# Performance work log

Hardware: AMD Instinct MI355X
Metric: run time of the kernel (lower is better)

The kernel has to match this reference:

```python
import jax, jax.numpy as jnp
import numpy as np

E = 1024      # emb_dim
H = 16        # num_heads
DH = E // H   # per-head atten_dim
B = 2
T = 2048


def _layernorm(x, scale, shift, eps=1e-5):
    mean = x.mean(axis=-1, keepdims=True)
    var = ((x - mean) ** 2).mean(axis=-1, keepdims=True)  # unbiased=False
    return scale * (x - mean) / jnp.sqrt(var + eps) + shift


def _gelu(x):
    # Faithful to source: tanh(sqrt(2/pi)*x + 0.044715*x^3)  (no sqrt on cubic term)
    c = jnp.sqrt(jnp.asarray(2.0 / jnp.pi, x.dtype))
    return 0.5 * x * (1.0 + jnp.tanh(c * x + 0.044715 * x ** 3))


def setup_inputs() -> dict:
    key = jax.random.key(0)
    ks = jax.random.split(key, 12)
    s = 0.02
    return {
        "x":     jax.random.normal(ks[0], (B, T, E), jnp.float32),
        "Wq":    jax.random.normal(ks[1], (H, E, DH), jnp.float32) * s,
        "Wk":    jax.random.normal(ks[2], (H, E, DH), jnp.float32) * s,
        "Wv":    jax.random.normal(ks[3], (H, E, DH), jnp.float32) * s,
        "fc_w":  jax.random.normal(ks[4], (E, E), jnp.float32) * s,
        "fc_b":  jnp.zeros((E,), jnp.float32),
        "ln1_s": jnp.ones((E,), jnp.float32),
        "ln1_b": jnp.zeros((E,), jnp.float32),
        "ln2_s": jnp.ones((E,), jnp.float32),
        "ln2_b": jnp.zeros((E,), jnp.float32),
        "ff_w1": jax.random.normal(ks[5], (E, 4 * E), jnp.float32) * s,
        "ff_b1": jnp.zeros((4 * E,), jnp.float32),
        "ff_w2": jax.random.normal(ks[6], (4 * E, E), jnp.float32) * s,
        "ff_b2": jnp.zeros((E,), jnp.float32),
    }


def _attention(x, Wq, Wk, Wv, fc_w, fc_b):
    b, t, _ = x.shape
    q = jnp.einsum("bte,hed->bhtd", x, Wq)
    k = jnp.einsum("bte,hed->bhtd", x, Wk)
    v = jnp.einsum("bte,hed->bhtd", x, Wv)
    scores = jnp.einsum("bhtd,bhsd->bhts", q, k)
    causal = jnp.triu(jnp.ones((t, t), bool), 1)
    scores = jnp.where(causal, -jnp.inf, scores)
    w = jax.nn.softmax(scores / jnp.sqrt(jnp.asarray(DH, x.dtype)), axis=-1)
    ctx = jnp.einsum("bhts,bhsd->bhtd", w, v)
    # faithful quirk from source: per-head transpose(1,2) then reshape(b, T, d_out)
    ctx = jnp.swapaxes(ctx, 2, 3).reshape(b, H, t, DH)
    concat = ctx.transpose(0, 2, 1, 3).reshape(b, t, E)
    return concat @ fc_w + fc_b


def reference(x, Wq, Wk, Wv, fc_w, fc_b, ln1_s, ln1_b, ln2_s, ln2_b,
              ff_w1, ff_b1, ff_w2, ff_b2):
    h = _attention(_layernorm(x, ln1_s, ln1_b), Wq, Wk, Wv, fc_w, fc_b) + x
    y = _layernorm(h, ln2_s, ln2_b)
    y = _gelu(y @ ff_w1 + ff_b1) @ ff_w2 + ff_b2
    return y + h
```

## Files before the change

kernel.cpp:

```cpp
#include <hip/hip_runtime.h>


#define En 1024
#define Hn 16
#define DHn 64
#define Bn 2
#define Tn 2048
#define Mrows 4096

typedef __attribute__((ext_vector_type(8))) short bf16x8;
typedef __attribute__((ext_vector_type(4))) float f32x4;

__device__ __forceinline__ short f2bf(float f) {
    unsigned u = __float_as_uint(f);
    u += 0x7FFFu + ((u >> 16) & 1u);
    return (short)(u >> 16);
}
__device__ __forceinline__ ushort f2bfu(float f) {
    unsigned u = __float_as_uint(f);
    u += 0x7FFFu + ((u >> 16) & 1u);
    return (ushort)(u >> 16);
}
__device__ __forceinline__ float bf2f(ushort u) {
    return __uint_as_float((unsigned)u << 16);
}
__device__ __forceinline__ unsigned cvt_pk_bf16(float lo, float hi) {
    unsigned r;
    asm("v_cvt_pk_bf16_f32 %0, %1, %2" : "=v"(r) : "v"(lo), "v"(hi));
    return r;
}

__device__ __forceinline__ float gelu_f(float x) {
    float u = 0.79788456080286535588f * x + 0.044715f * x * x * x;
    float t = __expf(2.0f * u);
    return x * t / (t + 1.0f);
}

__device__ __forceinline__ void load_lds16(const void* g, void* l) {
    __builtin_amdgcn_global_load_lds(
        (const __attribute__((address_space(1))) unsigned int*)(uintptr_t)g,
        (__attribute__((address_space(3))) unsigned int*)(uintptr_t)l,
        16, 0, 0);
}

__global__ __launch_bounds__(256) void ln_kernel(
    const float* __restrict__ in, const float* __restrict__ sc,
    const float* __restrict__ sh, ushort* __restrict__ out)
{
    int row = blockIdx.x;
    int tid = threadIdx.x;
    float4 v = ((const float4*)(in + (size_t)row * En))[tid];
    float s  = v.x + v.y + v.z + v.w;
    float s2 = v.x*v.x + v.y*v.y + v.z*v.z + v.w*v.w;
    #pragma unroll
    for (int off = 32; off > 0; off >>= 1) {
        s  += __shfl_down(s,  off);
        s2 += __shfl_down(s2, off);
    }
    __shared__ float red[2][4];
    int wave = tid >> 6, lane = tid & 63;
    if (lane == 0) { red[0][wave] = s; red[1][wave] = s2; }
    __syncthreads();
    s  = red[0][0] + red[0][1] + red[0][2] + red[0][3];
    s2 = red[1][0] + red[1][1] + red[1][2] + red[1][3];
    float mean = s * (1.0f / En);
    float var  = s2 * (1.0f / En) - mean * mean;
    float r = rsqrtf(var + 1e-5f);
    float4 scv = ((const float4*)sc)[tid];
    float4 shv = ((const float4*)sh)[tid];
    ushort4 o;
    o.x = f2bfu(scv.x * (v.x - mean) * r + shv.x);
    o.y = f2bfu(scv.y * (v.y - mean) * r + shv.y);
    o.z = f2bfu(scv.z * (v.z - mean) * r + shv.z);
    o.w = f2bfu(scv.w * (v.w - mean) * r + shv.w);
    ((ushort4*)(out + (size_t)row * En))[tid] = o;
}

__global__ __launch_bounds__(256) void ln2_fuse(
    const ushort* __restrict__ P0, const ushort* __restrict__ P1,
    const float* __restrict__ bias, const float* __restrict__ x,
    const float* __restrict__ sc, const float* __restrict__ sh,
    ushort* __restrict__ hb, ushort* __restrict__ ynb)
{
    int row = blockIdx.x, tid = threadIdx.x;
    size_t idx = (size_t)row * 256 + tid;
    ushort4 a = ((const ushort4*)P0)[idx];
    ushort4 b = ((const ushort4*)P1)[idx];
    float4 bi = ((const float4*)bias)[tid];
    float4 xr = ((const float4*)x)[idx];
    float4 v;
    v.x = bf2f(a.x) + bf2f(b.x) + bi.x + xr.x;
    v.y = bf2f(a.y) + bf2f(b.y) + bi.y + xr.y;
    v.z = bf2f(a.z) + bf2f(b.z) + bi.z + xr.z;
    v.w = bf2f(a.w) + bf2f(b.w) + bi.w + xr.w;
    ushort4 hv;
    hv.x = f2bfu(v.x); hv.y = f2bfu(v.y); hv.z = f2bfu(v.z); hv.w = f2bfu(v.w);
    ((ushort4*)hb)[idx] = hv;
    float s  = v.x + v.y + v.z + v.w;
    float s2 = v.x*v.x + v.y*v.y + v.z*v.z + v.w*v.w;
    #pragma unroll
    for (int off = 32; off > 0; off >>= 1) {
        s  += __shfl_down(s,  off);
        s2 += __shfl_down(s2, off);
    }
    __shared__ float red[2][4];
    int wave = tid >> 6, lane = tid & 63;
    if (lane == 0) { red[0][wave] = s; red[1][wave] = s2; }
    __syncthreads();
    s  = red[0][0] + red[0][1] + red[0][2] + red[0][3];
    s2 = red[1][0] + red[1][1] + red[1][2] + red[1][3];
    float mean = s * (1.0f / En);
    float var  = s2 * (1.0f / En) - mean * mean;
    float r = rsqrtf(var + 1e-5f);
    float4 scv = ((const float4*)sc)[tid];
    float4 shv = ((const float4*)sh)[tid];
    ushort4 o;
    o.x = f2bfu(scv.x * (v.x - mean) * r + shv.x);
    o.y = f2bfu(scv.y * (v.y - mean) * r + shv.y);
    o.z = f2bfu(scv.z * (v.z - mean) * r + shv.z);
    o.w = f2bfu(scv.w * (v.w - mean) * r + shv.w);
    ((ushort4*)ynb)[idx] = o;
}

__global__ __launch_bounds__(256) void ff2_reduce4(
    const ushort* __restrict__ P, const float* __restrict__ bias,
    const ushort* __restrict__ hb, float* __restrict__ out)
{
    int tid = threadIdx.x;
    size_t i = (size_t)blockIdx.x * 256 + tid;
    const size_t S = (size_t)Mrows * En / 4;
    ushort4 a = ((const ushort4*)P)[i];
    ushort4 b = ((const ushort4*)P)[i + S];
    ushort4 c = ((const ushort4*)P)[i + 2 * S];
    ushort4 d = ((const ushort4*)P)[i + 3 * S];
    float4 bi = ((const float4*)bias)[tid];
    ushort4 hu = ((const ushort4*)hb)[i];
    float4 o;
    o.x = (bf2f(a.x) + bf2f(b.x)) + (bf2f(c.x) + bf2f(d.x)) + bi.x + bf2f(hu.x);
    o.y = (bf2f(a.y) + bf2f(b.y)) + (bf2f(c.y) + bf2f(d.y)) + bi.y + bf2f(hu.y);
    o.z = (bf2f(a.z) + bf2f(b.z)) + (bf2f(c.z) + bf2f(d.z)) + bi.z + bf2f(hu.z);
    o.w = (bf2f(a.w) + bf2f(b.w)) + (bf2f(c.w) + bf2f(d.w)) + bi.w + bf2f(hu.w);
    ((float4*)out)[i] = o;
}

__global__ __launch_bounds__(256) void prep_w(
    const float* __restrict__ Wq, const float* __restrict__ Wk,
    const float* __restrict__ Wv, const float* __restrict__ fc_w,
    const float* __restrict__ ff_w1, const float* __restrict__ ff_w2,
    ushort* __restrict__ wqkv, ushort* __restrict__ wfc,
    ushort* __restrict__ wf1, ushort* __restrict__ wf2)
{
    int bid = blockIdx.x;
    const float* in; ushort* out; int N, ldo, k0, n0;
    if (bid < 768) {
        int z = bid >> 4, kb = bid & 15;
        int sel = z / 16, h = z % 16;
        in  = (sel == 0 ? Wq : sel == 1 ? Wk : Wv) + (size_t)h * En * DHn;
        out = wqkv + (size_t)(sel * 1024 + h * 64) * En;
        N = DHn; ldo = En; k0 = kb * 64; n0 = 0;
    } else if (bid < 1024) {
        int b2 = bid - 768;
        in = fc_w; out = wfc; N = En; ldo = En;
        k0 = (b2 & 15) * 64; n0 = (b2 >> 4) * 64;
    } else if (bid < 2048) {
        int b2 = bid - 1024;
        in = ff_w1; out = wf1; N = 4 * En; ldo = En;
        k0 = (b2 & 15) * 64; n0 = (b2 >> 4) * 64;
    } else {
        int b2 = bid - 2048;
        in = ff_w2; out = wf2; N = En; ldo = 4 * En;
        k0 = (b2 & 63) * 64; n0 = (b2 >> 6) * 64;
    }
    __shared__ float t[64][65];
    int tid = threadIdx.x, r = tid >> 4, c4 = (tid & 15) * 4;
    #pragma unroll
    for (int i = 0; i < 4; ++i) {
        float4 v = *(const float4*)(in + (size_t)(k0 + r + i * 16) * N + n0 + c4);
        t[r + i * 16][c4 + 0] = v.x; t[r + i * 16][c4 + 1] = v.y;
        t[r + i * 16][c4 + 2] = v.z; t[r + i * 16][c4 + 3] = v.w;
    }
    __syncthreads();
    #pragma unroll
    for (int i = 0; i < 4; ++i) {
        int n = r + i * 16;
        ushort4 u;
        u.x = f2bfu(t[c4 + 0][n]); u.y = f2bfu(t[c4 + 1][n]);
        u.z = f2bfu(t[c4 + 2][n]); u.w = f2bfu(t[c4 + 3][n]);
        *(ushort4*)(out + (size_t)(n0 + n) * ldo + k0 + c4) = u;
    }
}

template<int MODE, int TN>
__global__ __launch_bounds__(256) void gemm_bf16(
    const ushort* __restrict__ A, int lda,
    const ushort* __restrict__ Bt, int ldb, int Kloop,
    const float* __restrict__ bias,
    ushort* __restrict__ Cb, int ldc,
    ushort* __restrict__ qo, ushort* __restrict__ ko, ushort* __restrict__ vo)
{
    constexpr int WCN = TN / 2;
    constexpr int NI  = WCN / 16;
    constexpr int BIW = TN * 8 / 256;
    constexpr int STAGE = 128 * 64 + TN * 64;
    constexpr int BOUNCE = (MODE == 2 || MODE == 1) ? 4 * 64 * 68
                         : (MODE == 3 ? 128 * 68 : 0);
    constexpr int SMEMN = STAGE > BOUNCE ? STAGE : BOUNCE;
    __shared__ ushort smem[SMEMN];
    ushort* As = smem;
    ushort* Bs = smem + 128 * 64;
    int tid = threadIdx.x, wv = tid >> 6, lid = tid & 63;
    int m0 = blockIdx.x * 128, n0 = blockIdx.y * TN;
    int koff = blockIdx.z * Kloop;
    int wr = wv >> 1, wc = wv & 1;
    int hm = lid & 15, hk = lid >> 4;

    f32x4 acc[4][NI];
    #pragma unroll
    for (int i = 0; i < 4; ++i)
        #pragma unroll
        for (int j = 0; j < NI; ++j) acc[i][j] = (f32x4){0.f, 0.f, 0.f, 0.f};

    const ushort* Abase = A + (size_t)m0 * lda + koff;
    const ushort* Bbase = Bt + (size_t)n0 * ldb + koff;

    for (int k0 = 0; k0 < Kloop; k0 += 64) {
        __syncthreads();
        #pragma unroll
        for (int i = 0; i < 4; ++i) {
            int c = wv * 256 + i * 64 + lid;
            int r = c >> 3, s = c & 7;
            int j = s ^ (r & 7);
            load_lds16(Abase + (size_t)r * lda + k0 + j * 8,
                       &As[(wv * 256 + i * 64) * 8]);
        }
        #pragma unroll
        for (int i = 0; i < BIW; ++i) {
            int c = wv * (BIW * 64) + i * 64 + lid;
            int r = c >> 3, s = c & 7;
            int j = s ^ (r & 7);
            load_lds16(Bbase + (size_t)r * ldb + k0 + j * 8,
                       &Bs[(wv * (BIW * 64) + i * 64) * 8]);
        }
        __syncthreads();
        #pragma unroll
        for (int kk = 0; kk < 2; ++kk) {
            bf16x8 af[4], bfr[NI];
            #pragma unroll
            for (int mi = 0; mi < 4; ++mi) {
                int r = wr * 64 + mi * 16 + hm;
                int slot = ((kk << 2) | hk) ^ (r & 7);
                af[mi] = *(const bf16x8*)&As[(r * 8 + slot) * 8];
            }
            #pragma unroll
            for (int ni = 0; ni < NI; ++ni) {
                int r = wc * WCN + ni * 16 + hm;
                int slot = ((kk << 2) | hk) ^ (r & 7);
                bfr[ni] = *(const bf16x8*)&Bs[(r * 8 + slot) * 8];
            }
            #pragma unroll
            for (int mi = 0; mi < 4; ++mi)
                #pragma unroll
                for (int ni = 0; ni < NI; ++ni)
                    acc[mi][ni] = __builtin_amdgcn_mfma_f32_16x16x32_bf16(
                        af[mi], bfr[ni], acc[mi][ni], 0, 0, 0);
        }
    }

    int colbase = n0 + wc * WCN + hm;
    if (MODE == 1) {
        __syncthreads();
        ushort* Ls = smem + wv * (64 * 68);
        #pragma unroll
        for (int ni = 0; ni < NI; ++ni) {
            int col = colbase + ni * 16;
            float bb = bias[col];
            #pragma unroll
            for (int mi = 0; mi < 4; ++mi)
                #pragma unroll
                for (int r = 0; r < 4; ++r)
                    Ls[(mi * 16 + hk * 4 + r) * 68 + ni * 16 + hm] =
                        f2bfu(gelu_f(acc[mi][ni][r] + bb));
        }
        ushort* outp = Cb + (size_t)(m0 + wr * 64) * ldc + n0 + wc * 64;
        int dcol = hm * 4;
        #pragma unroll
        for (int i = 0; i < 16; ++i) {
            int t = hk + i * 4;
            *(ushort4*)(outp + (size_t)t * ldc + dcol) =
                *(const ushort4*)&Ls[t * 68 + dcol];
        }
    } else if (MODE == 2) {
        __syncthreads();
        ushort* Ls = smem + wv * (64 * 68);
        int col0 = n0 + wc * 64;
        int sel = col0 >> 10, h = (col0 & 1023) >> 6;
        if (sel < 2) {
            #pragma unroll
            for (int ni = 0; ni < NI; ++ni)
                #pragma unroll
                for (int mi = 0; mi < 4; ++mi)
                    #pragma unroll
                    for (int r = 0; r < 4; ++r)
                        Ls[(mi * 16 + hk * 4 + r) * 68 + ni * 16 + hm] =
                            f2bfu(acc[mi][ni][r]);
            ushort* outp = (sel == 0 ? qo : ko) + (size_t)h * (Mrows * DHn);
            int dcol = hm * 4;
            #pragma unroll
            for (int i = 0; i < 16; ++i) {
                int t = hk + i * 4;
                *(ushort4*)(outp + (size_t)(m0 + wr * 64 + t) * DHn + dcol) =
                    *(const ushort4*)&Ls[t * 68 + dcol];
            }
        } else {
            #pragma unroll
            for (int ni = 0; ni < NI; ++ni)
                #pragma unroll
                for (int mi = 0; mi < 4; ++mi)
                    #pragma unroll
                    for (int r = 0; r < 4; ++r)
                        Ls[(ni * 16 + hm) * 68 + mi * 16 + hk * 4 + r] =
                            f2bfu(acc[mi][ni][r]);
            int bb2 = m0 >> 11;
            int t0 = (m0 & 2047) + wr * 64;
            ushort* outp = vo + ((size_t)((h * 2 + bb2) * 64)) * Tn + t0;
            int tcol = hm * 4;
            #pragma unroll
            for (int i = 0; i < 16; ++i) {
                int d = hk + i * 4;
                *(ushort4*)(outp + (size_t)d * Tn + tcol) =
                    *(const ushort4*)&Ls[d * 68 + tcol];
            }
        }
    } else {
        __syncthreads();
        ushort* Ls = smem;
        #pragma unroll
        for (int ni = 0; ni < NI; ++ni)
            #pragma unroll
            for (int mi = 0; mi < 4; ++mi)
                #pragma unroll
                for (int r = 0; r < 4; ++r)
                    Ls[(wr * 64 + mi * 16 + hk * 4 + r) * 68
                       + wc * WCN + ni * 16 + hm] = f2bfu(acc[mi][ni][r]);
        __syncthreads();
        ushort* Cp = Cb + (size_t)blockIdx.z * Mrows * ldc;
        #pragma unroll
        for (int it = 0; it < 8; ++it) {
            int i = it * 1024 + tid * 4;
            int row = i >> 6, col = i & 63;
            *(ushort4*)(Cp + (size_t)(m0 + row) * ldc + n0 + col) =
                *(const ushort4*)&Ls[row * 68 + col];
        }
    }
}

#define MFMA_HALF(MH, KK) \
    _Pragma("unroll") \
    for (int mi = 0; mi < 4; ++mi) \
        _Pragma("unroll") \
        for (int ni = 0; ni < 4; ++ni) \
            acc[(MH) * 4 + mi][ni] = __builtin_amdgcn_mfma_f32_16x16x32_bf16( \
                af[MH][KK][mi], bfr[KK][ni], acc[(MH) * 4 + mi][ni], 0, 0, 0);

#define STAGE_A(bufp, h, ksrc) do { \
    ushort* _d = smem + (bufp) * 32768; \
    load_lds16(Abase + aoff[h][0] + (ksrc), _d + ldsoff[h][0]); \
    load_lds16(Abase + aoff[h][1] + (ksrc), _d + ldsoff[h][1]); \
} while (0)

#define STAGE_B(bufp, h, ksrc) do { \
    ushort* _d = smem + (bufp) * 32768 + 16384; \
    load_lds16(Bbase + boff[h][0] + (ksrc), _d + ldsoff[h][0]); \
    load_lds16(Bbase + boff[h][1] + (ksrc), _d + ldsoff[h][1]); \
} while (0)

template<int MODE, int SCHED>
__global__ __launch_bounds__(512, 2) void gemm256(
    const ushort* __restrict__ A, int lda,
    const ushort* __restrict__ Bt, int ldb, int Kloop,
    const float* __restrict__ bias,
    ushort* __restrict__ Cb, int ldc,
    ushort* __restrict__ qo, ushort* __restrict__ ko, ushort* __restrict__ vo)
{
    __shared__ ushort smem[65536];
    int tid = threadIdx.x, wv = tid >> 6, lid = tid & 63;
    int wr = wv >> 2, wc = wv & 3;
    int hm = lid & 15, hk = lid >> 4;
    int m0 = blockIdx.x * 256, n0 = blockIdx.y * 256;
    int koff = blockIdx.z * Kloop;
    int NT = Kloop >> 6;

    const ushort* Abase = A + (size_t)m0 * lda + koff;
    const ushort* Bbase = Bt + (size_t)n0 * ldb + koff;

    int aoff[2][2], boff[2][2], ldsoff[2][2];
    #pragma unroll
    for (int h = 0; h < 2; ++h)
        #pragma unroll
        for (int i = 0; i < 2; ++i) {
            int c = h * 1024 + wv * 128 + i * 64 + lid;
            int r = c >> 3, s = c & 7, j = s ^ (r & 7);
            aoff[h][i] = r * lda + j * 8;
            boff[h][i] = r * ldb + j * 8;
            ldsoff[h][i] = (h * 1024 + wv * 128 + i * 64) * 8;
        }

    int offA[2][2][4], offB[2][4];
    #pragma unroll
    for (int mh = 0; mh < 2; ++mh)
        #pragma unroll
        for (int kk = 0; kk < 2; ++kk)
            #pragma unroll
            for (int mi = 0; mi < 4; ++mi) {
                int r = wr * 128 + mh * 64 + mi * 16 + hm;
                offA[mh][kk][mi] = (r * 8 + (((kk << 2) | hk) ^ (r & 7))) * 8;
            }
    #pragma unroll
    for (int kk = 0; kk < 2; ++kk)
        #pragma unroll
        for (int ni = 0; ni < 4; ++ni) {
            int r = wc * 64 + ni * 16 + hm;
            offB[kk][ni] = (r * 8 + (((kk << 2) | hk) ^ (r & 7))) * 8;
        }

    f32x4 acc[8][4];
    #pragma unroll
    for (int i = 0; i < 8; ++i)
        #pragma unroll
        for (int j = 0; j < 4; ++j) acc[i][j] = (f32x4){0.f, 0.f, 0.f, 0.f};

    STAGE_A(0, 0, 0); STAGE_A(0, 1, 0);
    STAGE_B(0, 0, 0); STAGE_B(0, 1, 0);
    {
        int k1 = (NT > 1 ? 1 : 0) << 6;
        STAGE_B(1, 0, k1); STAGE_B(1, 1, k1);
    }
    asm volatile("s_waitcnt vmcnt(4)" ::: "memory");
    __builtin_amdgcn_s_barrier();

    for (int t = 0; t < NT; ++t) {
        int cur = t & 1, nxt = cur ^ 1;
        int kA = (t + 1 < NT ? t + 1 : NT - 1) << 6;
        int kB = (t + 2 < NT ? t + 2 : NT - 1) << 6;
        const ushort* As_ = smem + cur * 32768;
        const ushort* Bs_ = As_ + 16384;

        bf16x8 af[2][2][4], bfr[2][4];
        #pragma unroll
        for (int kk = 0; kk < 2; ++kk) {
            #pragma unroll
            for (int ni = 0; ni < 4; ++ni)
                bfr[kk][ni] = *(const bf16x8*)&Bs_[offB[kk][ni]];
            #pragma unroll
            for (int mh = 0; mh < 2; ++mh)
                #pragma unroll
                for (int mi = 0; mi < 4; ++mi)
                    af[mh][kk][mi] = *(const bf16x8*)&As_[offA[mh][kk][mi]];
        }
        STAGE_A(nxt, 0, kA);
        STAGE_A(nxt, 1, kA);
        if (SCHED == 1)
            asm volatile("s_waitcnt lgkmcnt(0)" ::: "memory");
        __builtin_amdgcn_s_setprio(1);
        MFMA_HALF(0, 0);
        MFMA_HALF(0, 1);
        __builtin_amdgcn_s_setprio(0);
        if (SCHED == 2)
            __builtin_amdgcn_sched_barrier(0);
        __builtin_amdgcn_s_barrier();

        STAGE_B(cur, 0, kB);
        STAGE_B(cur, 1, kB);
        __builtin_amdgcn_s_setprio(1);
        MFMA_HALF(1, 0);
        MFMA_HALF(1, 1);
        __builtin_amdgcn_s_setprio(0);
        if (SCHED == 2)
            __builtin_amdgcn_sched_barrier(0);
        asm volatile("s_waitcnt vmcnt(4)" ::: "memory");
        __builtin_amdgcn_s_barrier();
    }
    asm volatile("s_waitcnt vmcnt(0) lgkmcnt(0)" ::: "memory");
    __builtin_amdgcn_s_barrier();

    ushort* Ls = smem + wv * (64 * 68);
    int dcol = hm * 4;
    if (MODE == 1) {
        float bb[4];
        #pragma unroll
        for (int ni = 0; ni < 4; ++ni) bb[ni] = bias[n0 + wc * 64 + ni * 16 + hm];
        #pragma unroll
        for (int mh = 0; mh < 2; ++mh) {
            #pragma unroll
            for (int ni = 0; ni < 4; ++ni)
                #pragma unroll
                for (int mi = 0; mi < 4; ++mi)
                    #pragma unroll
                    for (int r = 0; r < 4; ++r)
                        Ls[(mi * 16 + hk * 4 + r) * 68 + ni * 16 + hm] =
                            f2bfu(gelu_f(acc[mh * 4 + mi][ni][r] + bb[ni]));
            ushort* outp = Cb + (size_t)(m0 + wr * 128 + mh * 64) * ldc
                              + n0 + wc * 64;
            #pragma unroll
            for (int i = 0; i < 16; ++i) {
                int tt = hk + i * 4;
                *(ushort4*)(outp + (size_t)tt * ldc + dcol) =
                    *(const ushort4*)&Ls[tt * 68 + dcol];
            }
        }
    } else if (MODE == 2) {
        int col0 = n0 + wc * 64;
        int sel = col0 >> 10, hh = (col0 & 1023) >> 6;
        #pragma unroll
        for (int mh = 0; mh < 2; ++mh) {
            int rowb = m0 + wr * 128 + mh * 64;
            if (sel < 2) {
                #pragma unroll
                for (int ni = 0; ni < 4; ++ni)
                    #pragma unroll
                    for (int mi = 0; mi < 4; ++mi)
                        #pragma unroll
                        for (int r = 0; r < 4; ++r)
                            Ls[(mi * 16 + hk * 4 + r) * 68 + ni * 16 + hm] =
                                f2bfu(acc[mh * 4 + mi][ni][r]);
                ushort* outp = (sel == 0 ? qo : ko) + (size_t)hh * (Mrows * DHn);
                #pragma unroll
                for (int i = 0; i < 16; ++i) {
                    int tt = hk + i * 4;
                    *(ushort4*)(outp + (size_t)(rowb + tt) * DHn + dcol) =
                        *(const ushort4*)&Ls[tt * 68 + dcol];
                }
            } else {
                #pragma unroll
                for (int ni = 0; ni < 4; ++ni)
                    #pragma unroll
                    for (int mi = 0; mi < 4; ++mi)
                        #pragma unroll
                        for (int r = 0; r < 4; ++r)
                            Ls[(ni * 16 + hm) * 68 + mi * 16 + hk * 4 + r] =
                                f2bfu(acc[mh * 4 + mi][ni][r]);
                int bb2 = m0 >> 11;
                int t0 = (m0 & 2047) + wr * 128 + mh * 64;
                ushort* outp = vo + ((size_t)((hh * 2 + bb2) * 64)) * Tn + t0;
                #pragma unroll
                for (int i = 0; i < 16; ++i) {
                    int d = hk + i * 4;
                    *(ushort4*)(outp + (size_t)d * Tn + dcol) =
                        *(const ushort4*)&Ls[d * 68 + dcol];
                }
            }
        }
    } else {
        ushort* Cp = Cb + (size_t)blockIdx.z * ((size_t)Mrows * ldc);
        #pragma unroll
        for (int mh = 0; mh < 2; ++mh) {
            #pragma unroll
            for (int ni = 0; ni < 4; ++ni)
                #pragma unroll
                for (int mi = 0; mi < 4; ++mi)
                    #pragma unroll
                    for (int r = 0; r < 4; ++r)
                        Ls[(mi * 16 + hk * 4 + r) * 68 + ni * 16 + hm] =
                            f2bfu(acc[mh * 4 + mi][ni][r]);
            ushort* outp = Cp + (size_t)(m0 + wr * 128 + mh * 64) * ldc
                              + n0 + wc * 64;
            #pragma unroll
            for (int i = 0; i < 16; ++i) {
                int tt = hk + i * 4;
                *(ushort4*)(outp + (size_t)tt * ldc + dcol) =
                    *(const ushort4*)&Ls[tt * 68 + dcol];
            }
        }
    }
}

__global__ __launch_bounds__(512) void attn_mfma(
    const ushort* __restrict__ q, const ushort* __restrict__ ksrc,
    const ushort* __restrict__ vtsrc, ushort* __restrict__ cat)
{
    int g = blockIdx.x;
    int h = g >> 1, b = g & 1;
    const ushort* qg  = q     + (size_t)g * Tn * DHn;
    const ushort* kg  = ksrc  + (size_t)g * Tn * DHn;
    const ushort* vtg = vtsrc + (size_t)g * DHn * Tn;
    int tid = threadIdx.x, w = tid >> 6, lane = tid & 63;
    int m = lane & 15, gq = lane >> 4;
    int qoff = gq * 4;

    __shared__ short Ks[2][2][4096];
    __shared__ short Vt[2][2][4096];
    __shared__ short Ps[8][1024];

    int R = tid >> 3;
    int c = tid & 7;
    int slot = R * 64 + ((c ^ (R & 7)) << 3);
    const ushort* kbase = kg  + (size_t)R * DHn + c * 8;
    const ushort* vbase = vtg + (size_t)R * Tn  + c * 8;

    #pragma unroll 1
    for (int phase = 0; phase < 2; ++phase) {
        int qj = phase ? (15 - (int)blockIdx.y) : (int)blockIdx.y;
        int q0 = qj * 128;
        int NR = qj + 1;
        int qb = q0 + w * 16;

        bf16x8 qf[2];
        {
            const ushort* qp = qg + (size_t)(qb + m) * DHn + gq * 8;
            qf[0] = *(const bf16x8*)(qp);
            qf[1] = *(const bf16x8*)(qp + 32);
        }
        f32x4 o[4];
        #pragma unroll
        for (int i = 0; i < 4; ++i) o[i] = (f32x4){0.f, 0.f, 0.f, 0.f};
        float lsum = 0.f;

        {
            bf16x8 a0 = *(const bf16x8*)(kbase);
            bf16x8 a1 = *(const bf16x8*)(kbase + 4096);
            bf16x8 b0 = *(const bf16x8*)(vbase);
            bf16x8 b1 = *(const bf16x8*)(vbase + 64);
            *(bf16x8*)&Ks[0][0][slot] = a0;
            *(bf16x8*)&Ks[0][1][slot] = a1;
            *(bf16x8*)&Vt[0][0][slot] = b0;
            *(bf16x8*)&Vt[0][1][slot] = b1;
        }
        __syncthreads();

        #pragma unroll 1
        for (int rd = 0; rd < NR; ++rd) {
            int cur = rd & 1;
            bf16x8 k0r, k1r, v0r, v1r;
            bool pre = (rd + 1 < NR);
            if (pre) {
                k0r = *(const bf16x8*)(kbase + (size_t)(2 * rd + 2) * 4096);
                k1r = *(const bf16x8*)(kbase + (size_t)(2 * rd + 3) * 4096);
                v0r = *(const bf16x8*)(vbase + (2 * rd + 2) * 64);
                v1r = *(const bf16x8*)(vbase + (2 * rd + 3) * 64);
            }
            #pragma unroll
            for (int hf = 0; hf < 2; ++hf) {
                int kt = 2 * rd + hf;
                const short* Kt_ = &Ks[cur][hf][0];
                const short* Vt_ = &Vt[cur][hf][0];
                if (qb < kt * 64) continue;

                #pragma unroll
                for (int ct = 0; ct < 4; ++ct) {
                    int dk2 = kt * 64 + ct * 16 - qb;
                    uint2 u;
                    if (dk2 > 0) {
                        u.x = 0u; u.y = 0u;
                    } else {
                        f32x4 acc = (f32x4){0.f, 0.f, 0.f, 0.f};
                        int row = ct * 16 + m;
                        __builtin_amdgcn_s_setprio(1);
                        #pragma unroll
                        for (int db = 0; db < 2; ++db) {
                            bf16x8 kf = *(const bf16x8*)
                                &Kt_[row * 64 + (((db * 4 + gq) ^ (row & 7)) << 3)];
                            acc = __builtin_amdgcn_mfma_f32_16x16x32_bf16(
                                kf, qf[db], acc, 0, 0, 0);
                        }
                        __builtin_amdgcn_s_setprio(0);
                        float p0, p1, p2, p3;
                        if (dk2 == 0) {
                            p0 = (qoff + 0 > m) ? 0.f : __expf(acc[0] * 0.125f);
                            p1 = (qoff + 1 > m) ? 0.f : __expf(acc[1] * 0.125f);
                            p2 = (qoff + 2 > m) ? 0.f : __expf(acc[2] * 0.125f);
                            p3 = (qoff + 3 > m) ? 0.f : __expf(acc[3] * 0.125f);
                        } else {
                            p0 = __expf(acc[0] * 0.125f);
                            p1 = __expf(acc[1] * 0.125f);
                            p2 = __expf(acc[2] * 0.125f);
                            p3 = __expf(acc[3] * 0.125f);
                        }
                        lsum += (p0 + p1) + (p2 + p3);
                        u.x = cvt_pk_bf16(p0, p1);
                        u.y = cvt_pk_bf16(p2, p3);
                    }
                    *(uint2*)&Ps[w][m * 64 +
                        (((ct * 2 + (gq >> 1)) ^ (m & 7)) << 3) + ((gq & 1) << 2)] = u;
                }

                bf16x8 pf0 = *(const bf16x8*)
                    &Ps[w][m * 64 + ((gq ^ (m & 7)) << 3)];
                bf16x8 pf1 = *(const bf16x8*)
                    &Ps[w][m * 64 + (((4 + gq) ^ (m & 7)) << 3)];
                __builtin_amdgcn_s_setprio(1);
                #pragma unroll
                for (int ct2 = 0; ct2 < 4; ++ct2) {
                    int row = ct2 * 16 + m;
                    bf16x8 vf0 = *(const bf16x8*)
                        &Vt_[row * 64 + ((gq ^ (row & 7)) << 3)];
                    o[ct2] = __builtin_amdgcn_mfma_f32_16x16x32_bf16(
                        pf0, vf0, o[ct2], 0, 0, 0);
                    bf16x8 vf1 = *(const bf16x8*)
                        &Vt_[row * 64 + (((4 + gq) ^ (row & 7)) << 3)];
                    o[ct2] = __builtin_amdgcn_mfma_f32_16x16x32_bf16(
                        pf1, vf1, o[ct2], 0, 0, 0);
                }
                __builtin_amdgcn_s_setprio(0);
            }
            if (pre) {
                int nb = cur ^ 1;
                *(bf16x8*)&Ks[nb][0][slot] = k0r;
                *(bf16x8*)&Ks[nb][1][slot] = k1r;
                *(bf16x8*)&Vt[nb][0][slot] = v0r;
                *(bf16x8*)&Vt[nb][1][slot] = v1r;
            }
            __syncthreads();
        }

        float l = lsum;
        l += __shfl_xor(l, 16);
        l += __shfl_xor(l, 32);
        float inv[4];
        #pragma unroll
        for (int r = 0; r < 4; ++r)
            inv[r] = 1.0f / __shfl(l, qoff + r);

        int qt_old = (q0 >> 6) + (w >> 2);
        int wv_old = w & 3;
        size_t base = (size_t)b * Tn * En + (size_t)h * 64 + (size_t)qt_old * En
                    + wv_old * 16 + gq * 4;
        #pragma unroll
        for (int ct2 = 0; ct2 < 4; ++ct2) {
            int d = ct2 * 16 + m;
            #pragma unroll
            for (int r = 0; r < 4; ++r)
                cat[base + (size_t)d * 32 * En + r] = f2bfu(o[ct2][r] * inv[r]);
        }
    }
}

extern "C" void kernel_launch(void* const* d_in, const int* in_sizes, int n_in,
                              void* d_out, int out_size, void* d_ws, size_t ws_size,
                              hipStream_t stream) {
    const float* x     = (const float*)d_in[0];
    const float* Wq    = (const float*)d_in[1];
    const float* Wk    = (const float*)d_in[2];
    const float* Wv    = (const float*)d_in[3];
    const float* fc_w  = (const float*)d_in[4];
    const float* fc_b  = (const float*)d_in[5];
    const float* ln1_s = (const float*)d_in[6];
    const float* ln1_b = (const float*)d_in[7];
    const float* ln2_s = (const float*)d_in[8];
    const float* ln2_b = (const float*)d_in[9];
    const float* ff_w1 = (const float*)d_in[10];
    const float* ff_b1 = (const float*)d_in[11];
    const float* ff_w2 = (const float*)d_in[12];
    const float* ff_b2 = (const float*)d_in[13];
    float* out = (float*)d_out;
    (void)in_sizes; (void)n_in; (void)out_size; (void)ws_size;

    const size_t MB = 1048576;
    char* w8 = (char*)d_ws;
    ushort* S0   = (ushort*)(w8 + 0 * MB);
    ushort* kb   = (ushort*)(w8 + 8 * MB);
    ushort* vtb  = (ushort*)(w8 + 16 * MB);
    ushort* qb   = (ushort*)(w8 + 24 * MB);
    ushort* hb   = (ushort*)(w8 + 32 * MB);
    ushort* Pfc  = (ushort*)(w8 + 48 * MB);
    ushort* y1   = (ushort*)(w8 + 48 * MB);
    ushort* Pff2 = (ushort*)(w8 + 0 * MB);
    ushort* wqkv = (ushort*)(w8 + 80 * MB);
    ushort* wfc  = (ushort*)(w8 + 86 * MB);
    ushort* wf1  = (ushort*)(w8 + 88 * MB);
    ushort* wf2  = (ushort*)(w8 + 96 * MB);

    prep_w<<<dim3(3072), 256, 0, stream>>>(
        Wq, Wk, Wv, fc_w, ff_w1, ff_w2, wqkv, wfc, wf1, wf2);

    ln_kernel<<<dim3(Mrows), 256, 0, stream>>>(x, ln1_s, ln1_b, S0);
    gemm256<2, 2><<<dim3(16, 12), 512, 0, stream>>>(
        S0, En, wqkv, En, En, nullptr, nullptr, 0, qb, kb, vtb);
    attn_mfma<<<dim3(Hn * Bn, 8), 512, 0, stream>>>(qb, kb, vtb, S0);
    gemm_bf16<3, 64><<<dim3(32, 16, 2), 256, 0, stream>>>(
        S0, En, wfc, En, En / 2, nullptr, Pfc, En, nullptr, nullptr, nullptr);
    ln2_fuse<<<dim3(Mrows), 256, 0, stream>>>(
        Pfc, Pfc + (size_t)Mrows * En, fc_b, x, ln2_s, ln2_b, hb, qb);
    gemm256<1, 2><<<dim3(16, 16), 512, 0, stream>>>(
        qb, En, wf1, En, En, ff_b1, y1, 4 * En, nullptr, nullptr, nullptr);
    gemm256<3, 1><<<dim3(16, 4, 4), 512, 0, stream>>>(
        y1, 4 * En, wf2, 4 * En, En, nullptr, Pff2, En, nullptr, nullptr, nullptr);
    ff2_reduce4<<<dim3(Mrows), 256, 0, stream>>>(Pff2, ff_b2, hb, out);
}
```

Baseline: 309.6 us.

## Shrink attention blocks to 64-query tiles and unify GEMM scheduling

The attention kernel moves from 512-thread blocks covering 128 query rows to 256-thread blocks covering 64 query rows, with twice as many blocks along y. Each thread now loads two 16-byte K/V chunks. The causal pairing of query tiles is kept at the new granularity. Smaller blocks give finer causal load balance and less wasted work on the diagonal, at the cost of re-streaming K/V tiles more often. Separately, the GEMM template drops its SCHED parameter, so every GEMM now always waits on lgkmcnt and no longer uses sched_barrier, which changes the QKV and FF1 schedules.

```diff
diff --git a/kernel.cpp b/kernel.cpp
--- a/kernel.cpp
+++ b/kernel.cpp
@@ -374,7 +374,7 @@
     load_lds16(Bbase + boff[h][1] + (ksrc), _d + ldsoff[h][1]); \
 } while (0)
 
-template<int MODE, int SCHED>
+template<int MODE>
 __global__ __launch_bounds__(512, 2) void gemm256(
     const ushort* __restrict__ A, int lda,
     const ushort* __restrict__ Bt, int ldb, int Kloop,
@@ -459,14 +459,11 @@
         }
         STAGE_A(nxt, 0, kA);
         STAGE_A(nxt, 1, kA);
-        if (SCHED == 1)
-            asm volatile("s_waitcnt lgkmcnt(0)" ::: "memory");
+        asm volatile("s_waitcnt lgkmcnt(0)" ::: "memory");
         __builtin_amdgcn_s_setprio(1);
         MFMA_HALF(0, 0);
         MFMA_HALF(0, 1);
         __builtin_amdgcn_s_setprio(0);
-        if (SCHED == 2)
-            __builtin_amdgcn_sched_barrier(0);
         __builtin_amdgcn_s_barrier();
 
         STAGE_B(cur, 0, kB);
@@ -475,8 +472,6 @@
         MFMA_HALF(1, 0);
         MFMA_HALF(1, 1);
         __builtin_amdgcn_s_setprio(0);
-        if (SCHED == 2)
-            __builtin_amdgcn_sched_barrier(0);
         asm volatile("s_waitcnt vmcnt(4)" ::: "memory");
         __builtin_amdgcn_s_barrier();
     }
@@ -574,7 +569,7 @@
     }
 }
 
-__global__ __launch_bounds__(512) void attn_mfma(
+__global__ __launch_bounds__(256) void attn_mfma(
     const ushort* __restrict__ q, const ushort* __restrict__ ksrc,
     const ushort* __restrict__ vtsrc, ushort* __restrict__ cat)
 {
@@ -589,19 +584,21 @@
 
     __shared__ short Ks[2][2][4096];
     __shared__ short Vt[2][2][4096];
-    __shared__ short Ps[8][1024];
-
-    int R = tid >> 3;
-    int c = tid & 7;
-    int slot = R * 64 + ((c ^ (R & 7)) << 3);
-    const ushort* kbase = kg  + (size_t)R * DHn + c * 8;
-    const ushort* vbase = vtg + (size_t)R * Tn  + c * 8;
+    __shared__ short Ps[4][1024];
+
+    int R = tid >> 2;
+    int c2 = tid & 3;
+    int slot0 = R * 64 + (((c2 * 2    ) ^ (R & 7)) << 3);
+    int slot1 = R * 64 + (((c2 * 2 + 1) ^ (R & 7)) << 3);
+    const ushort* kbase = kg  + (size_t)R * DHn + c2 * 16;
+    const ushort* vbase = vtg + (size_t)R * Tn  + c2 * 16;
 
     #pragma unroll 1
     for (int phase = 0; phase < 2; ++phase) {
-        int qj = phase ? (15 - (int)blockIdx.y) : (int)blockIdx.y;
-        int q0 = qj * 128;
-        int NR = qj + 1;
+        int qt = phase ? (31 - (int)blockIdx.y) : (int)blockIdx.y;
+        int q0 = qt * 64;
+        int NTt = qt + 1;
+        int NR = (NTt + 1) >> 1;
         int qb = q0 + w * 16;
 
         bf16x8 qf[2];
@@ -617,26 +614,38 @@
 
         {
             bf16x8 a0 = *(const bf16x8*)(kbase);
-            bf16x8 a1 = *(const bf16x8*)(kbase + 4096);
+            bf16x8 a1 = *(const bf16x8*)(kbase + 8);
+            bf16x8 a2 = *(const bf16x8*)(kbase + 4096);
+            bf16x8 a3 = *(const bf16x8*)(kbase + 4096 + 8);
             bf16x8 b0 = *(const bf16x8*)(vbase);
-            bf16x8 b1 = *(const bf16x8*)(vbase + 64);
-            *(bf16x8*)&Ks[0][0][slot] = a0;
-            *(bf16x8*)&Ks[0][1][slot] = a1;
-            *(bf16x8*)&Vt[0][0][slot] = b0;
-            *(bf16x8*)&Vt[0][1][slot] = b1;
+            bf16x8 b1 = *(const bf16x8*)(vbase + 8);
+            bf16x8 b2 = *(const bf16x8*)(vbase + 64);
+            bf16x8 b3 = *(const bf16x8*)(vbase + 64 + 8);
+            *(bf16x8*)&Ks[0][0][slot0] = a0;
+            *(bf16x8*)&Ks[0][0][slot1] = a1;
+            *(bf16x8*)&Ks[0][1][slot0] = a2;
+            *(bf16x8*)&Ks[0][1][slot1] = a3;
+            *(bf16x8*)&Vt[0][0][slot0] = b0;
+            *(bf16x8*)&Vt[0][0][slot1] = b1;
+            *(bf16x8*)&Vt[0][1][slot0] = b2;
+            *(bf16x8*)&Vt[0][1][slot1] = b3;
         }
         __syncthreads();
 
         #pragma unroll 1
         for (int rd = 0; rd < NR; ++rd) {
             int cur = rd & 1;
-            bf16x8 k0r, k1r, v0r, v1r;
+            bf16x8 kr[4], vr[4];
             bool pre = (rd + 1 < NR);
             if (pre) {
-                k0r = *(const bf16x8*)(kbase + (size_t)(2 * rd + 2) * 4096);
-                k1r = *(const bf16x8*)(kbase + (size_t)(2 * rd + 3) * 4096);
-                v0r = *(const bf16x8*)(vbase + (2 * rd + 2) * 64);
-                v1r = *(const bf16x8*)(vbase + (2 * rd + 3) * 64);
+                const ushort* kp2 = kbase + (size_t)(2 * rd + 2) * 4096;
+                const ushort* kp3 = kbase + (size_t)(2 * rd + 3) * 4096;
+                const ushort* vp2 = vbase + (2 * rd + 2) * 64;
+                const ushort* vp3 = vbase + (2 * rd + 3) * 64;
+                kr[0] = *(const bf16x8*)(kp2); kr[1] = *(const bf16x8*)(kp2 + 8);
+                kr[2] = *(const bf16x8*)(kp3); kr[3] = *(const bf16x8*)(kp3 + 8);
+                vr[0] = *(const bf16x8*)(vp2); vr[1] = *(const bf16x8*)(vp2 + 8);
+                vr[2] = *(const bf16x8*)(vp3); vr[3] = *(const bf16x8*)(vp3 + 8);
             }
             #pragma unroll
             for (int hf = 0; hf < 2; ++hf) {
@@ -704,10 +713,14 @@
             }
             if (pre) {
                 int nb = cur ^ 1;
-                *(bf16x8*)&Ks[nb][0][slot] = k0r;
-                *(bf16x8*)&Ks[nb][1][slot] = k1r;
-                *(bf16x8*)&Vt[nb][0][slot] = v0r;
-                *(bf16x8*)&Vt[nb][1][slot] = v1r;
+                *(bf16x8*)&Ks[nb][0][slot0] = kr[0];
+                *(bf16x8*)&Ks[nb][0][slot1] = kr[1];
+                *(bf16x8*)&Ks[nb][1][slot0] = kr[2];
+                *(bf16x8*)&Ks[nb][1][slot1] = kr[3];
+                *(bf16x8*)&Vt[nb][0][slot0] = vr[0];
+                *(bf16x8*)&Vt[nb][0][slot1] = vr[1];
+                *(bf16x8*)&Vt[nb][1][slot0] = vr[2];
+                *(bf16x8*)&Vt[nb][1][slot1] = vr[3];
             }
             __syncthreads();
         }
@@ -720,10 +733,8 @@
         for (int r = 0; r < 4; ++r)
             inv[r] = 1.0f / __shfl(l, qoff + r);
 
-        int qt_old = (q0 >> 6) + (w >> 2);
-        int wv_old = w & 3;
-        size_t base = (size_t)b * Tn * En + (size_t)h * 64 + (size_t)qt_old * En
-                    + wv_old * 16 + gq * 4;
+        size_t base = (size_t)b * Tn * En + (size_t)h * 64 + (size_t)qt * En
+                    + w * 16 + gq * 4;
         #pragma unroll
         for (int ct2 = 0; ct2 < 4; ++ct2) {
             int d = ct2 * 16 + m;
@@ -773,16 +784,16 @@
         Wq, Wk, Wv, fc_w, ff_w1, ff_w2, wqkv, wfc, wf1, wf2);
 
     ln_kernel<<<dim3(Mrows), 256, 0, stream>>>(x, ln1_s, ln1_b, S0);
-    gemm256<2, 2><<<dim3(16, 12), 512, 0, stream>>>(
+    gemm256<2><<<dim3(16, 12), 512, 0, stream>>>(
         S0, En, wqkv, En, En, nullptr, nullptr, 0, qb, kb, vtb);
-    attn_mfma<<<dim3(Hn * Bn, 8), 512, 0, stream>>>(qb, kb, vtb, S0);
+    attn_mfma<<<dim3(Hn * Bn, 16), 256, 0, stream>>>(qb, kb, vtb, S0);
     gemm_bf16<3, 64><<<dim3(32, 16, 2), 256, 0, stream>>>(
         S0, En, wfc, En, En / 2, nullptr, Pfc, En, nullptr, nullptr, nullptr);
     ln2_fuse<<<dim3(Mrows), 256, 0, stream>>>(
         Pfc, Pfc + (size_t)Mrows * En, fc_b, x, ln2_s, ln2_b, hb, qb);
-    gemm256<1, 2><<<dim3(16, 16), 512, 0, stream>>>(
+    gemm256<1><<<dim3(16, 16), 512, 0, stream>>>(
         qb, En, wf1, En, En, ff_b1, y1, 4 * En, nullptr, nullptr, nullptr);
-    gemm256<3, 1><<<dim3(16, 4, 4), 512, 0, stream>>>(
+    gemm256<3><<<dim3(16, 4, 4), 512, 0, stream>>>(
         y1, 4 * En, wf2, 4 * En, En, nullptr, Pff2, En, nullptr, nullptr, nullptr);
     ff2_reduce4<<<dim3(Mrows), 256, 0, stream>>>(Pff2, ff_b2, hb, out);
 }
```

After: 321.0 us. 1.04x slower.
